# Optimization experiments

Hardware: AMD Instinct MI355X
Metric: run time of the kernel (lower is better)

The kernel has to match this reference:

```python
import jax, jax.numpy as jnp
import numpy as np

N = 100000      # nodes
E = 1600000     # edges (before self-loops)
F_IN = 16       # num_node_features
HID = 16        # hid
HEADS = 4       # in_head == out_head
B = 64          # num graphs
G = 16          # num_global_features
NEG_SLOPE = 0.2


def gat_conv(x, src, dst, W, a_src, a_dst, b, concat):
    """PyG-style GATConv. x:[N,F], W:[F,H*C], a_src/a_dst:[H,C], b:[H*C] or [C]."""
    n = x.shape[0]
    H, C = a_src.shape
    h = (x @ W).reshape(n, H, C)                       # [N,H,C]
    alpha_s = (h * a_src).sum(-1)                      # [N,H]
    alpha_d = (h * a_dst).sum(-1)                      # [N,H]
    e = jax.nn.leaky_relu(alpha_s[src] + alpha_d[dst], NEG_SLOPE)  # [E',H]
    # segment softmax over destination nodes (stable; max is grad-free)
    m = jax.lax.stop_gradient(jax.ops.segment_max(e, dst, num_segments=n))
    ex = jnp.exp(e - m[dst])
    denom = jax.ops.segment_sum(ex, dst, num_segments=n)
    alpha = ex / (denom[dst] + 1e-16)                  # [E',H]
    out = jax.ops.segment_sum(h[src] * alpha[:, :, None], dst, num_segments=n)  # [N,H,C]
    out = out.reshape(n, H * C) if concat else out.mean(axis=1)
    return out + b


def setup_inputs() -> dict:
    key = jax.random.key(0)
    ks = jax.random.split(key, 24)
    s = 0.1
    inp = {
        "x": jax.random.normal(ks[0], (N, F_IN), jnp.float32),
        "stats": jax.random.normal(ks[1], (B, G), jnp.float32),
        # conv1: F_IN -> HID, heads=HEADS, concat=True
        "W1": jax.random.normal(ks[2], (F_IN, HEADS * HID), jnp.float32) * s,
        "a1s": jax.random.normal(ks[3], (HEADS, HID), jnp.float32) * s,
        "a1d": jax.random.normal(ks[4], (HEADS, HID), jnp.float32) * s,
        "b1": jnp.zeros((HEADS * HID,), jnp.float32),
        # conv2: HID*HEADS -> HID, heads=HEADS, concat=False
        "W2": jax.random.normal(ks[5], (HEADS * HID, HEADS * HID), jnp.float32) * s,
        "a2s": jax.random.normal(ks[6], (HEADS, HID), jnp.float32) * s,
        "a2d": jax.random.normal(ks[7], (HEADS, HID), jnp.float32) * s,
        "b2": jnp.zeros((HID,), jnp.float32),
        # conv3: HID -> HID, heads=HEADS, concat=False
        "W3": jax.random.normal(ks[8], (HID, HEADS * HID), jnp.float32) * s,
        "a3s": jax.random.normal(ks[9], (HEADS, HID), jnp.float32) * s,
        "a3d": jax.random.normal(ks[10], (HEADS, HID), jnp.float32) * s,
        "b3": jnp.zeros((HID,), jnp.float32),
        # MLP head
        "fw1": jax.random.normal(ks[11], (HID + G, 32), jnp.float32) * s,
        "fb1": jnp.zeros((32,), jnp.float32),
        "fw2": jax.random.normal(ks[12], (32, 16), jnp.float32) * s,
        "fb2": jnp.zeros((16,), jnp.float32),
        "fw3": jax.random.normal(ks[13], (16, 1), jnp.float32) * s,
        "fb3": jnp.zeros((1,), jnp.float32),
        "edge_index": jax.random.randint(ks[14], (2, E), 0, N, jnp.int64),
        "batch": jnp.sort(jax.random.randint(ks[15], (N,), 0, B, jnp.int64)),
    }
    return inp


def reference(x, stats, W1, a1s, a1d, b1, W2, a2s, a2d, b2, W3, a3s, a3d, b3,
              fw1, fb1, fw2, fb2, fw3, fb3, edge_index, batch):
    n = x.shape[0]
    loops = jnp.arange(n, dtype=edge_index.dtype)
    src = jnp.concatenate([edge_index[0], loops])  # add_self_loops=True (PyG default)
    dst = jnp.concatenate([edge_index[1], loops])
    h = jax.nn.elu(gat_conv(x, src, dst, W1, a1s, a1d, b1, True))
    h = jax.nn.elu(gat_conv(h, src, dst, W2, a2s, a2d, b2, False))
    h = gat_conv(h, src, dst, W3, a3s, a3d, b3, False)
    nb = stats.shape[0]
    pooled = jax.ops.segment_sum(h, batch, num_segments=nb)
    counts = jax.ops.segment_sum(jnp.ones((n,), h.dtype), batch, num_segments=nb)
    pooled = pooled / jnp.maximum(counts, 1.0)[:, None]   # global_mean_pool
    z = jnp.concatenate([pooled, stats], axis=1)
    z = jax.nn.relu(z @ fw1 + fb1)
    z = jax.nn.relu(z @ fw2 + fb2)
    return z @ fw3 + fb3
```

## Files before the change

### kernel.cpp

```cpp
#include <hip/hip_runtime.h>
#include <hip/hip_bf16.h>
#include <hip/hip_fp16.h>

#define NNODES 100000
#define NEDGES 1600000
#define NB     64
#define NG     16
#define POOL_SLOTS (NB * NG + NB)

#define BKT_SHIFT 7
#define NPB 128
#define NBKT ((NNODES + NPB - 1) / NPB)
#define BCAP 4096
#define SCAT_BLOCKS 256
#define NL1_BLOCKS 2048
#define REC 128

typedef float vf2 __attribute__((ext_vector_type(2)));

__device__ __forceinline__ float leaky02(float v) {
    return v > 0.0f ? v : 0.2f * v;
}

__device__ __forceinline__ unsigned char cvt_fp8(float a) {
    int r = __builtin_amdgcn_cvt_pk_fp8_f32(a, a, 0, false);
    return (unsigned char)(r & 0xFF);
}

__device__ __forceinline__ float4 loadQ4(const unsigned char* p) {
    int u = *(const int*)p;
    vf2 lo = __builtin_amdgcn_cvt_pk_f32_fp8(u, false);
    vf2 hi = __builtin_amdgcn_cvt_pk_f32_fp8(u, true);
    return make_float4(lo.x, lo.y, hi.x, hi.y);
}

__device__ __forceinline__ void storeH4(__half* p, float4 v) {
    __half2 a = __floats2half2_rn(v.x, v.y);
    __half2 b = __floats2half2_rn(v.z, v.w);
    uint2 raw;
    raw.x = *reinterpret_cast<unsigned*>(&a);
    raw.y = *reinterpret_cast<unsigned*>(&b);
    *(uint2*)p = raw;
}

template <int FIN>
__device__ __forceinline__ void nl_body_f32(const float* __restrict__ X,
                                            const float* __restrict__ W,
                                            const float* __restrict__ a_s,
                                            const float* __restrict__ a_d,
                                            unsigned char* __restrict__ Hrec,
                                            float* __restrict__ AD, int n,
                                            int wave0, int nwaves, int lane) {
    int head = lane >> 4;
    float w[FIN];
#pragma unroll
    for (int k = 0; k < FIN; ++k) w[k] = W[k * 64 + lane];
    float asl = a_s[lane], adl = a_d[lane];

    for (int i = wave0; i < n; i += nwaves) {
        const float* __restrict__ xr = X + (size_t)i * FIN;
        float acc = 0.0f;
#pragma unroll
        for (int k = 0; k < FIN; ++k) acc += xr[k] * w[k];
        unsigned char* row = Hrec + (size_t)i * REC;
        row[lane] = cvt_fp8(acc);
        float s1 = acc * asl, s2 = acc * adl;
#pragma unroll
        for (int off = 1; off < 16; off <<= 1) {
            s1 += __shfl_xor(s1, off);
            s2 += __shfl_xor(s2, off);
        }
        if ((lane & 15) == 0) {
            ((float*)(row + 64))[head] = s1;
            AD[(size_t)i * 4 + head] = s2;
        }
    }
}

template <int FIN>
__global__ void node_linear3h(const unsigned* __restrict__ X,
                              const float* __restrict__ W,
                              const float* __restrict__ a_s,
                              const float* __restrict__ a_d,
                              unsigned char* __restrict__ Hrec,
                              float* __restrict__ AD, int n) {
    int lane = threadIdx.x & 63;
    int head = lane >> 4;
    int wave = __builtin_amdgcn_readfirstlane(
        (int)((blockIdx.x * blockDim.x + threadIdx.x) >> 6));
    int nwaves = (gridDim.x * blockDim.x) >> 6;

    float w[FIN];
#pragma unroll
    for (int k = 0; k < FIN; ++k) w[k] = W[k * 64 + lane];
    float asl = a_s[lane], adl = a_d[lane];

    for (int i = wave; i < n; i += nwaves) {
        const unsigned* __restrict__ xr = X + (size_t)i * (FIN / 2);
        float acc = 0.0f;
#pragma unroll
        for (int k = 0; k < FIN / 2; ++k) {
            unsigned u = xr[k];
            __half2 hh = *reinterpret_cast<const __half2*>(&u);
            float2 f = __half22float2(hh);
            acc += f.x * w[2 * k] + f.y * w[2 * k + 1];
        }
        unsigned char* row = Hrec + (size_t)i * REC;
        row[lane] = cvt_fp8(acc);
        float s1 = acc * asl, s2 = acc * adl;
#pragma unroll
        for (int off = 1; off < 16; off <<= 1) {
            s1 += __shfl_xor(s1, off);
            s2 += __shfl_xor(s2, off);
        }
        if ((lane & 15) == 0) {
            ((float*)(row + 64))[head] = s1;
            AD[(size_t)i * 4 + head] = s2;
        }
    }
}

__global__ void scatter_nl1(const int* __restrict__ src,
                            const int* __restrict__ dst,
                            int* __restrict__ bucketCnt,
                            unsigned int* __restrict__ pairs, int ne,
                            const float* __restrict__ X,
                            const float* __restrict__ W,
                            const float* __restrict__ a_s,
                            const float* __restrict__ a_d,
                            unsigned char* __restrict__ Hrec,
                            float* __restrict__ AD, int n) {
    __shared__ int hist[NBKT];
    __shared__ int base[NBKT];
    int tid = threadIdx.x;

    if (blockIdx.x >= SCAT_BLOCKS) {
        int lane = tid & 63;
        int wave = __builtin_amdgcn_readfirstlane(
            (int)(((blockIdx.x - SCAT_BLOCKS) * blockDim.x + tid) >> 6));
        int nwaves = (NL1_BLOCKS * 256) >> 6;
        nl_body_f32<16>(X, W, a_s, a_d, Hrec, AD, n, wave, nwaves, lane);
        return;
    }

    for (int i = tid; i < NBKT; i += 256) hist[i] = 0;
    __syncthreads();

    int chunk = (ne + SCAT_BLOCKS - 1) / SCAT_BLOCKS;
    int beg = blockIdx.x * chunk;
    int end = min(beg + chunk, ne);

    for (int e0 = beg; e0 < end; e0 += 1024) {
        int d[4];
#pragma unroll
        for (int q = 0; q < 4; ++q) {
            int e = e0 + q * 256 + tid;
            d[q] = (e < end) ? dst[e] : -1;
        }
#pragma unroll
        for (int q = 0; q < 4; ++q)
            if (d[q] >= 0) atomicAdd(&hist[d[q] >> BKT_SHIFT], 1);
    }
    __syncthreads();

    for (int i = tid; i < NBKT; i += 256) {
        int h = hist[i];
        base[i] = h ? atomicAdd(&bucketCnt[i], h) : 0;
        hist[i] = 0;
    }
    __syncthreads();

    for (int e0 = beg; e0 < end; e0 += 1024) {
        int d[4], s[4];
#pragma unroll
        for (int q = 0; q < 4; ++q) {
            int e = e0 + q * 256 + tid;
            d[q] = (e < end) ? dst[e] : -1;
            s[q] = (e < end) ? src[e] : 0;
        }
        int r[4], bkt[4];
#pragma unroll
        for (int q = 0; q < 4; ++q) {
            if (d[q] >= 0) {
                bkt[q] = d[q] >> BKT_SHIFT;
                r[q] = base[bkt[q]] + atomicAdd(&hist[bkt[q]], 1);
            }
        }
#pragma unroll
        for (int q = 0; q < 4; ++q) {
            if (d[q] >= 0 && r[q] < BCAP)
                pairs[(size_t)bkt[q] * BCAP + r[q]] =
                    (unsigned)s[q] | ((unsigned)(d[q] & (NPB - 1)) << 20);
        }
    }
}

__global__ void bucket_sort(const unsigned int* __restrict__ pairs,
                            const int* __restrict__ bucketCnt,
                            int* __restrict__ srcs,
                            int* __restrict__ indptr, int n) {
    __shared__ int hist[NPB];
    __shared__ int offl[NPB];
    __shared__ int cur[NPB];
    __shared__ int red[256];
    __shared__ int lsrc[BCAP];
    int bkt = blockIdx.x;
    int t = threadIdx.x;
    int cnt = min(bucketCnt[bkt], BCAP);

    int partial = 0;
    for (int j = t; j < bkt; j += 256) partial += min(bucketCnt[j], BCAP);
    red[t] = partial;
    if (t < NPB) hist[t] = 0;
    __syncthreads();
    for (int s = 128; s > 0; s >>= 1) {
        if (t < s) red[t] += red[t + s];
        __syncthreads();
    }
    int boff = red[0];
    if (bkt == NBKT - 1 && t == 0) indptr[n] = boff + cnt;

    const unsigned int* __restrict__ p = pairs + (size_t)bkt * BCAP;
    unsigned int v[BCAP / 256];
#pragma unroll
    for (int i = 0; i < BCAP / 256; ++i) {
        int e = i * 256 + t;
        v[i] = 0u;
        if (e < cnt) {
            v[i] = p[e];
            atomicAdd(&hist[v[i] >> 20], 1);
        }
    }
    __syncthreads();
    if (t < NPB) offl[t] = hist[t];
    __syncthreads();
    for (int off = 1; off < NPB; off <<= 1) {
        int x = 0;
        if (t < NPB && t >= off) x = offl[t - off];
        __syncthreads();
        if (t < NPB && t >= off) offl[t] += x;
        __syncthreads();
    }
    if (t < NPB) {
        int ex = offl[t] - hist[t];
        cur[t] = ex;
        int node = bkt * NPB + t;
        if (node < n) indptr[node] = boff + ex;
    }
    __syncthreads();
#pragma unroll
    for (int i = 0; i < BCAP / 256; ++i) {
        int e = i * 256 + t;
        if (e < cnt) {
            int r = atomicAdd(&cur[v[i] >> 20], 1);
            lsrc[r] = (int)(v[i] & 0xFFFFFu);
        }
    }
    __syncthreads();
    for (int e = t; e < cnt; e += 256) srcs[boff + e] = lsrc[e];
}

__device__ __forceinline__ float4 gat_agg_core(
    const unsigned char* __restrict__ Hrec, const float* __restrict__ AD,
    const int* __restrict__ indptr, const int* __restrict__ srcs,
    int d, int grp, int sl, int head) {
    const unsigned char* __restrict__ rowD = Hrec + (size_t)d * REC;
    float ad  = AD[(size_t)d * 4 + head];
    float asd = *(const float*)(rowD + 64 + 4 * head);
    float t0 = asd + ad;
    float wself = __expf(leaky02(t0));
    float den = wself;
    float4 h4s = loadQ4(rowD + sl * 4);
    float4 acc = make_float4(wself * h4s.x, wself * h4s.y,
                             wself * h4s.z, wself * h4s.w);

    int beg = indptr[d], end = indptr[d + 1];
    for (int e0 = beg; e0 < end; e0 += 16) {
        int cnt = min(16, end - e0);
        int myS = (sl < cnt) ? srcs[e0 + sl] : 0;
        int j = 0;
        for (; j + 4 <= cnt; j += 4) {
            const unsigned char* r[4];
            float a[4]; float4 h4[4];
#pragma unroll
            for (int q = 0; q < 4; ++q) {
                int s = __shfl(myS, (grp << 4) + j + q);
                r[q] = Hrec + (size_t)s * REC;
            }
#pragma unroll
            for (int q = 0; q < 4; ++q)
                a[q] = *(const float*)(r[q] + 64 + 4 * head);
#pragma unroll
            for (int q = 0; q < 4; ++q) h4[q] = loadQ4(r[q] + sl * 4);
#pragma unroll
            for (int q = 0; q < 4; ++q) {
                float t = a[q] + ad;
                float w = __expf(leaky02(t));
                den += w;
                acc.x += w * h4[q].x; acc.y += w * h4[q].y;
                acc.z += w * h4[q].z; acc.w += w * h4[q].w;
            }
        }
        for (; j < cnt; ++j) {
            int s = __shfl(myS, (grp << 4) + j);
            const unsigned char* rr = Hrec + (size_t)s * REC;
            float t = *(const float*)(rr + 64 + 4 * head) + ad;
            float w = __expf(leaky02(t));
            float4 h4 = loadQ4(rr + sl * 4);
            den += w;
            acc.x += w * h4.x; acc.y += w * h4.y;
            acc.z += w * h4.z; acc.w += w * h4.w;
        }
    }
    float inv = 1.0f / (den + 1e-16f);
    return make_float4(acc.x * inv, acc.y * inv, acc.z * inv, acc.w * inv);
}

__global__ void gat_pull_l1(const unsigned char* __restrict__ Hrec,
                            const float* __restrict__ AD,
                            const int* __restrict__ indptr,
                            const int* __restrict__ srcs,
                            const float* __restrict__ bias,
                            __half* __restrict__ out, int n) {
    int lane = threadIdx.x & 63;
    int grp = lane >> 4, sl = lane & 15, head = sl >> 2;
    int wave = (blockIdx.x * blockDim.x + threadIdx.x) >> 6;
    int nwaves = (gridDim.x * blockDim.x) >> 6;
    for (int d0 = wave * 4; d0 < n; d0 += nwaves * 4) {
        int d = d0 + grp;
        if (d < n) {
            float4 v = gat_agg_core(Hrec, AD, indptr, srcs, d, grp, sl, head);
            float4 b4 = *(const float4*)(bias + sl * 4);
            v.x += b4.x; v.y += b4.y; v.z += b4.z; v.w += b4.w;
            v.x = v.x > 0.f ? v.x : __expf(v.x) - 1.f;
            v.y = v.y > 0.f ? v.y : __expf(v.y) - 1.f;
            v.z = v.z > 0.f ? v.z : __expf(v.z) - 1.f;
            v.w = v.w > 0.f ? v.w : __expf(v.w) - 1.f;
            storeH4(out + (size_t)d * 64 + sl * 4, v);
        }
    }
}

__global__ void gat_pull_l2(const unsigned char* __restrict__ Hrec,
                            float* __restrict__ AD,
                            const int* __restrict__ indptr,
                            const int* __restrict__ srcs,
                            const float* __restrict__ bias,
                            const float* __restrict__ W3,
                            const float* __restrict__ a3s,
                            const float* __restrict__ a3d,
                            unsigned char* __restrict__ Hout, int n) {
    __shared__ float w3s[16 * 64];
    for (int i = threadIdx.x; i < 16 * 64; i += 256) w3s[i] = W3[i];
    __syncthreads();

    int lane = threadIdx.x & 63;
    int grp = lane >> 4, sl = lane & 15, head = sl >> 2;
    int wave = (blockIdx.x * blockDim.x + threadIdx.x) >> 6;
    int nwaves = (gridDim.x * blockDim.x) >> 6;
    float4 as4 = *(const float4*)(a3s + head * 16 + (sl & 3) * 4);
    float4 ad4 = *(const float4*)(a3d + head * 16 + (sl & 3) * 4);
    float4 b4  = *(const float4*)(bias + (sl & 3) * 4);

    for (int d0 = wave * 4; d0 < n; d0 += nwaves * 4) {
        int d = d0 + grp;
        if (d < n) {
            float4 v = gat_agg_core(Hrec, AD, indptr, srcs, d, grp, sl, head);
#pragma unroll
            for (int off = 4; off <= 8; off <<= 1) {
                v.x += __shfl_xor(v.x, off);
                v.y += __shfl_xor(v.y, off);
                v.z += __shfl_xor(v.z, off);
                v.w += __shfl_xor(v.w, off);
            }
            v.x = 0.25f * v.x + b4.x; v.y = 0.25f * v.y + b4.y;
            v.z = 0.25f * v.z + b4.z; v.w = 0.25f * v.w + b4.w;
            v.x = v.x > 0.f ? v.x : __expf(v.x) - 1.f;
            v.y = v.y > 0.f ? v.y : __expf(v.y) - 1.f;
            v.z = v.z > 0.f ? v.z : __expf(v.z) - 1.f;
            v.w = v.w > 0.f ? v.w : __expf(v.w) - 1.f;

            float xin[16];
#pragma unroll
            for (int q = 0; q < 4; ++q) {
                int srcl = (grp << 4) + q;
                xin[4 * q + 0] = __shfl(v.x, srcl);
                xin[4 * q + 1] = __shfl(v.y, srcl);
                xin[4 * q + 2] = __shfl(v.z, srcl);
                xin[4 * q + 3] = __shfl(v.w, srcl);
            }
            float4 o = make_float4(0.f, 0.f, 0.f, 0.f);
#pragma unroll
            for (int k = 0; k < 16; ++k) {
                float4 wr = *(const float4*)&w3s[k * 64 + 4 * sl];
                o.x += xin[k] * wr.x; o.y += xin[k] * wr.y;
                o.z += xin[k] * wr.z; o.w += xin[k] * wr.w;
            }
            unsigned char* rowO = Hout + (size_t)d * REC;
            int pk = __builtin_amdgcn_cvt_pk_fp8_f32(o.x, o.y, 0, false);
            pk = __builtin_amdgcn_cvt_pk_fp8_f32(o.z, o.w, pk, true);
            *(int*)(rowO + 4 * sl) = pk;
            float s1 = o.x * as4.x + o.y * as4.y + o.z * as4.z + o.w * as4.w;
            float s2 = o.x * ad4.x + o.y * ad4.y + o.z * ad4.z + o.w * ad4.w;
            s1 += __shfl_xor(s1, 1); s1 += __shfl_xor(s1, 2);
            s2 += __shfl_xor(s2, 1); s2 += __shfl_xor(s2, 2);
            if ((sl & 3) == 0) {
                ((float*)(rowO + 64))[head] = s1;
                AD[(size_t)d * 4 + head] = s2;
            }
        }
    }
}

__global__ void gat_pull_l3(const unsigned char* __restrict__ Hrec,
                            const float* __restrict__ AD,
                            const int* __restrict__ indptr,
                            const int* __restrict__ srcs,
                            const float* __restrict__ bias,
                            const int* __restrict__ batch,
                            float* __restrict__ PC, int n) {
    __shared__ float lp[POOL_SLOTS];
    for (int i = threadIdx.x; i < POOL_SLOTS; i += 256) lp[i] = 0.f;
    __syncthreads();

    int lane = threadIdx.x & 63;
    int grp = lane >> 4, sl = lane & 15, head = sl >> 2;
    int wave = (blockIdx.x * blockDim.x + threadIdx.x) >> 6;
    int nwaves = (gridDim.x * blockDim.x) >> 6;
    float4 b4 = *(const float4*)(bias + (sl & 3) * 4);

    for (int d0 = wave * 4; d0 < n; d0 += nwaves * 4) {
        int d = d0 + grp;
        if (d < n) {
            float4 v = gat_agg_core(Hrec, AD, indptr, srcs, d, grp, sl, head);
#pragma unroll
            for (int off = 4; off <= 8; off <<= 1) {
                v.x += __shfl_xor(v.x, off);
                v.y += __shfl_xor(v.y, off);
                v.z += __shfl_xor(v.z, off);
                v.w += __shfl_xor(v.w, off);
            }
            v.x = 0.25f * v.x + b4.x; v.y = 0.25f * v.y + b4.y;
            v.z = 0.25f * v.z + b4.z; v.w = 0.25f * v.w + b4.w;
            if (sl < 4) {
                int b = batch[d];
                atomicAdd(&lp[b * 16 + sl * 4 + 0], v.x);
                atomicAdd(&lp[b * 16 + sl * 4 + 1], v.y);
                atomicAdd(&lp[b * 16 + sl * 4 + 2], v.z);
                atomicAdd(&lp[b * 16 + sl * 4 + 3], v.w);
                if (sl == 0) atomicAdd(&lp[NB * NG + b], 1.0f);
            }
        }
    }
    __syncthreads();
    for (int i = threadIdx.x; i < POOL_SLOTS; i += 256) {
        float s = lp[i];
        if (s != 0.f) atomicAdd(&PC[i], s);
    }
}

__global__ void mlp_head(const float* __restrict__ pooled_counts,
                         const float* __restrict__ stats,
                         const float* __restrict__ fw1, const float* __restrict__ fb1,
                         const float* __restrict__ fw2, const float* __restrict__ fb2,
                         const float* __restrict__ fw3, const float* __restrict__ fb3,
                         float* __restrict__ out) {
    int g = threadIdx.x;
    if (g >= NB) return;
    const float* pooled = pooled_counts;
    const float* counts = pooled_counts + NB * NG;
    float z[32];
    float inv = 1.0f / fmaxf(counts[g], 1.0f);
#pragma unroll
    for (int c = 0; c < 16; ++c) z[c] = pooled[g * 16 + c] * inv;
#pragma unroll
    for (int c = 0; c < 16; ++c) z[16 + c] = stats[g * 16 + c];

    float z1[32];
#pragma unroll
    for (int j = 0; j < 32; ++j) {
        float acc = fb1[j];
        for (int k = 0; k < 32; ++k) acc += z[k] * fw1[k * 32 + j];
        z1[j] = fmaxf(acc, 0.0f);
    }
    float z2[16];
#pragma unroll
    for (int j = 0; j < 16; ++j) {
        float acc = fb2[j];
        for (int k = 0; k < 32; ++k) acc += z1[k] * fw2[k * 16 + j];
        z2[j] = fmaxf(acc, 0.0f);
    }
    float acc = fb3[0];
#pragma unroll
    for (int k = 0; k < 16; ++k) acc += z2[k] * fw3[k];
    out[g] = acc;
}

extern "C" void kernel_launch(void* const* d_in, const int* in_sizes, int n_in,
                              void* d_out, int out_size, void* d_ws, size_t ws_size,
                              hipStream_t stream) {
    const float* x    = (const float*)d_in[0];
    const float* stats= (const float*)d_in[1];
    const float* W1   = (const float*)d_in[2];
    const float* a1s  = (const float*)d_in[3];
    const float* a1d  = (const float*)d_in[4];
    const float* b1   = (const float*)d_in[5];
    const float* W2   = (const float*)d_in[6];
    const float* a2s  = (const float*)d_in[7];
    const float* a2d  = (const float*)d_in[8];
    const float* b2   = (const float*)d_in[9];
    const float* W3   = (const float*)d_in[10];
    const float* a3s  = (const float*)d_in[11];
    const float* a3d  = (const float*)d_in[12];
    const float* b3   = (const float*)d_in[13];
    const float* fw1  = (const float*)d_in[14];
    const float* fb1  = (const float*)d_in[15];
    const float* fw2  = (const float*)d_in[16];
    const float* fb2  = (const float*)d_in[17];
    const float* fw3  = (const float*)d_in[18];
    const float* fb3  = (const float*)d_in[19];
    const int* ei     = (const int*)d_in[20];
    const int* batch  = (const int*)d_in[21];

    const int n = NNODES, ne = NEDGES;
    const int* srcI = ei;
    const int* dstI = ei + ne;

    unsigned char* HqA = (unsigned char*)d_ws;
    unsigned char* HqB = HqA + (size_t)n * REC;
    float* AD   = (float*)(HqB + (size_t)n * REC);
    float* PC   = AD + (size_t)n * 4;
    int* bucketCnt = (int*)(PC + POOL_SLOTS);
    int* indptr    = bucketCnt + NBKT;
    int* srcs      = indptr + (n + 1);
    size_t off = (size_t)((char*)(srcs + ne) - (char*)d_ws);
    off = (off + 255) & ~(size_t)255;
    unsigned int* pairs = (unsigned int*)((char*)d_ws + off);
    __half* B16 = (__half*)pairs;

    const int TB = 256;
    const int nlBlocks   = 2048;
    const int pullBlocks = (n + 15) / 16;

    hipMemsetAsync(PC, 0, (POOL_SLOTS + NBKT) * sizeof(int), stream);

    scatter_nl1<<<SCAT_BLOCKS + NL1_BLOCKS, TB, 0, stream>>>(
        srcI, dstI, bucketCnt, pairs, ne,
        x, W1, a1s, a1d, HqA, AD, n);
    bucket_sort<<<NBKT, TB, 0, stream>>>(pairs, bucketCnt, srcs, indptr, n);

    gat_pull_l1<<<pullBlocks, TB, 0, stream>>>(HqA, AD, indptr, srcs, b1, B16, n);

    node_linear3h<64><<<nlBlocks, TB, 0, stream>>>((const unsigned*)B16, W2,
                                                   a2s, a2d, HqA, AD, n);
    gat_pull_l2<<<pullBlocks, TB, 0, stream>>>(HqA, AD, indptr, srcs, b2,
                                               W3, a3s, a3d, HqB, n);
    gat_pull_l3<<<pullBlocks, TB, 0, stream>>>(HqB, AD, indptr, srcs, b3,
                                               batch, PC, n);

    mlp_head<<<1, 64, 0, stream>>>(PC, stats, fw1, fb1, fw2, fb2, fw3, fb3,
                                   (float*)d_out);
}
```

Before: 331.1 us.

## Split node records into packed fp8 features and separate alpha arrays, deepen gather unroll

Result: slower. 395.9 us (+19.6%).

```diff
diff --git a/kernel.cpp b/kernel.cpp
--- a/kernel.cpp
+++ b/kernel.cpp
@@ -14,7 +14,6 @@
 #define BCAP 4096
 #define SCAT_BLOCKS 256
 #define NL1_BLOCKS 2048
-#define REC 128
 
 typedef float vf2 __attribute__((ext_vector_type(2)));
 
@@ -48,7 +47,8 @@
                                             const float* __restrict__ W,
                                             const float* __restrict__ a_s,
                                             const float* __restrict__ a_d,
-                                            unsigned char* __restrict__ Hrec,
+                                            unsigned char* __restrict__ H,
+                                            float* __restrict__ AS,
                                             float* __restrict__ AD, int n,
                                             int wave0, int nwaves, int lane) {
     int head = lane >> 4;
@@ -62,8 +62,7 @@
         float acc = 0.0f;
 #pragma unroll
         for (int k = 0; k < FIN; ++k) acc += xr[k] * w[k];
-        unsigned char* row = Hrec + (size_t)i * REC;
-        row[lane] = cvt_fp8(acc);
+        H[(size_t)i * 64 + lane] = cvt_fp8(acc);
         float s1 = acc * asl, s2 = acc * adl;
 #pragma unroll
         for (int off = 1; off < 16; off <<= 1) {
@@ -71,7 +70,7 @@
             s2 += __shfl_xor(s2, off);
         }
         if ((lane & 15) == 0) {
-            ((float*)(row + 64))[head] = s1;
+            AS[(size_t)i * 4 + head] = s1;
             AD[(size_t)i * 4 + head] = s2;
         }
     }
@@ -82,7 +81,8 @@
                               const float* __restrict__ W,
                               const float* __restrict__ a_s,
                               const float* __restrict__ a_d,
-                              unsigned char* __restrict__ Hrec,
+                              unsigned char* __restrict__ H,
+                              float* __restrict__ AS,
                               float* __restrict__ AD, int n) {
     int lane = threadIdx.x & 63;
     int head = lane >> 4;
@@ -105,8 +105,7 @@
             float2 f = __half22float2(hh);
             acc += f.x * w[2 * k] + f.y * w[2 * k + 1];
         }
-        unsigned char* row = Hrec + (size_t)i * REC;
-        row[lane] = cvt_fp8(acc);
+        H[(size_t)i * 64 + lane] = cvt_fp8(acc);
         float s1 = acc * asl, s2 = acc * adl;
 #pragma unroll
         for (int off = 1; off < 16; off <<= 1) {
@@ -114,7 +113,7 @@
             s2 += __shfl_xor(s2, off);
         }
         if ((lane & 15) == 0) {
-            ((float*)(row + 64))[head] = s1;
+            AS[(size_t)i * 4 + head] = s1;
             AD[(size_t)i * 4 + head] = s2;
         }
     }
@@ -128,7 +127,8 @@
                             const float* __restrict__ W,
                             const float* __restrict__ a_s,
                             const float* __restrict__ a_d,
-                            unsigned char* __restrict__ Hrec,
+                            unsigned char* __restrict__ H,
+                            float* __restrict__ AS,
                             float* __restrict__ AD, int n) {
     __shared__ int hist[NBKT];
     __shared__ int base[NBKT];
@@ -139,7 +139,7 @@
         int wave = __builtin_amdgcn_readfirstlane(
             (int)(((blockIdx.x - SCAT_BLOCKS) * blockDim.x + tid) >> 6));
         int nwaves = (NL1_BLOCKS * 256) >> 6;
-        nl_body_f32<16>(X, W, a_s, a_d, Hrec, AD, n, wave, nwaves, lane);
+        nl_body_f32<16>(X, W, a_s, a_d, H, AS, AD, n, wave, nwaves, lane);
         return;
     }
 
@@ -155,7 +155,7 @@
 #pragma unroll
         for (int q = 0; q < 4; ++q) {
             int e = e0 + q * 256 + tid;
-            d[q] = (e < end) ? dst[e] : -1;
+            d[q] = (e < end) ? __builtin_nontemporal_load(dst + e) : -1;
         }
 #pragma unroll
         for (int q = 0; q < 4; ++q)
@@ -175,8 +175,8 @@
 #pragma unroll
         for (int q = 0; q < 4; ++q) {
             int e = e0 + q * 256 + tid;
-            d[q] = (e < end) ? dst[e] : -1;
-            s[q] = (e < end) ? src[e] : 0;
+            d[q] = (e < end) ? __builtin_nontemporal_load(dst + e) : -1;
+            s[q] = (e < end) ? __builtin_nontemporal_load(src + e) : 0;
         }
         int r[4], bkt[4];
 #pragma unroll
@@ -189,8 +189,9 @@
 #pragma unroll
         for (int q = 0; q < 4; ++q) {
             if (d[q] >= 0 && r[q] < BCAP)
-                pairs[(size_t)bkt[q] * BCAP + r[q]] =
-                    (unsigned)s[q] | ((unsigned)(d[q] & (NPB - 1)) << 20);
+                __builtin_nontemporal_store(
+                    (unsigned)s[q] | ((unsigned)(d[q] & (NPB - 1)) << 20),
+                    pairs + (size_t)bkt[q] * BCAP + r[q]);
         }
     }
 }
@@ -227,7 +228,7 @@
         int e = i * 256 + t;
         v[i] = 0u;
         if (e < cnt) {
-            v[i] = p[e];
+            v[i] = __builtin_nontemporal_load(p + e);
             atomicAdd(&hist[v[i] >> 20], 1);
         }
     }
@@ -261,37 +262,58 @@
 }
 
 __device__ __forceinline__ float4 gat_agg_core(
-    const unsigned char* __restrict__ Hrec, const float* __restrict__ AD,
+    const unsigned char* __restrict__ H, const float* __restrict__ AS,
+    const float* __restrict__ AD,
     const int* __restrict__ indptr, const int* __restrict__ srcs,
     int d, int grp, int sl, int head) {
-    const unsigned char* __restrict__ rowD = Hrec + (size_t)d * REC;
+    int beg = indptr[d], end = indptr[d + 1];
+    int myS = 0;
+    if (beg < end && sl < min(16, end - beg))
+        myS = __builtin_nontemporal_load(srcs + beg + sl);
+
     float ad  = AD[(size_t)d * 4 + head];
-    float asd = *(const float*)(rowD + 64 + 4 * head);
+    float asd = AS[(size_t)d * 4 + head];
     float t0 = asd + ad;
     float wself = __expf(leaky02(t0));
     float den = wself;
-    float4 h4s = loadQ4(rowD + sl * 4);
+    float4 h4s = loadQ4(H + (size_t)d * 64 + sl * 4);
     float4 acc = make_float4(wself * h4s.x, wself * h4s.y,
                              wself * h4s.z, wself * h4s.w);
 
-    int beg = indptr[d], end = indptr[d + 1];
     for (int e0 = beg; e0 < end; e0 += 16) {
         int cnt = min(16, end - e0);
-        int myS = (sl < cnt) ? srcs[e0 + sl] : 0;
         int j = 0;
+        for (; j + 8 <= cnt; j += 8) {
+            int s[8]; float a[8]; float4 h4[8];
+#pragma unroll
+            for (int q = 0; q < 8; ++q)
+                s[q] = __shfl(myS, (grp << 4) + j + q);
+#pragma unroll
+            for (int q = 0; q < 8; ++q)
+                a[q] = AS[(size_t)s[q] * 4 + head];
+#pragma unroll
+            for (int q = 0; q < 8; ++q)
+                h4[q] = loadQ4(H + (size_t)s[q] * 64 + sl * 4);
+#pragma unroll
+            for (int q = 0; q < 8; ++q) {
+                float t = a[q] + ad;
+                float w = __expf(leaky02(t));
+                den += w;
+                acc.x += w * h4[q].x; acc.y += w * h4[q].y;
+                acc.z += w * h4[q].z; acc.w += w * h4[q].w;
+            }
+        }
         for (; j + 4 <= cnt; j += 4) {
-            const unsigned char* r[4];
-            float a[4]; float4 h4[4];
-#pragma unroll
-            for (int q = 0; q < 4; ++q) {
-                int s = __shfl(myS, (grp << 4) + j + q);
-                r[q] = Hrec + (size_t)s * REC;
-            }
+            int s[4]; float a[4]; float4 h4[4];
 #pragma unroll
             for (int q = 0; q < 4; ++q)
-                a[q] = *(const float*)(r[q] + 64 + 4 * head);
-#pragma unroll
-            for (int q = 0; q < 4; ++q) h4[q] = loadQ4(r[q] + sl * 4);
+                s[q] = __shfl(myS, (grp << 4) + j + q);
+#pragma unroll
+            for (int q = 0; q < 4; ++q)
+                a[q] = AS[(size_t)s[q] * 4 + head];
+#pragma unroll
+            for (int q = 0; q < 4; ++q)
+                h4[q] = loadQ4(H + (size_t)s[q] * 64 + sl * 4);
 #pragma unroll
             for (int q = 0; q < 4; ++q) {
                 float t = a[q] + ad;
@@ -303,20 +325,23 @@
         }
         for (; j < cnt; ++j) {
             int s = __shfl(myS, (grp << 4) + j);
-            const unsigned char* rr = Hrec + (size_t)s * REC;
-            float t = *(const float*)(rr + 64 + 4 * head) + ad;
+            float t = AS[(size_t)s * 4 + head] + ad;
             float w = __expf(leaky02(t));
-            float4 h4 = loadQ4(rr + sl * 4);
+            float4 h4 = loadQ4(H + (size_t)s * 64 + sl * 4);
             den += w;
             acc.x += w * h4.x; acc.y += w * h4.y;
             acc.z += w * h4.z; acc.w += w * h4.w;
         }
+        int nb = e0 + 16;
+        if (nb < end && sl < min(16, end - nb))
+            myS = __builtin_nontemporal_load(srcs + nb + sl);
     }
     float inv = 1.0f / (den + 1e-16f);
     return make_float4(acc.x * inv, acc.y * inv, acc.z * inv, acc.w * inv);
 }
 
-__global__ void gat_pull_l1(const unsigned char* __restrict__ Hrec,
+__global__ void gat_pull_l1(const unsigned char* __restrict__ H,
+                            const float* __restrict__ AS,
                             const float* __restrict__ AD,
                             const int* __restrict__ indptr,
                             const int* __restrict__ srcs,
@@ -329,7 +354,7 @@
     for (int d0 = wave * 4; d0 < n; d0 += nwaves * 4) {
         int d = d0 + grp;
         if (d < n) {
-            float4 v = gat_agg_core(Hrec, AD, indptr, srcs, d, grp, sl, head);
+            float4 v = gat_agg_core(H, AS, AD, indptr, srcs, d, grp, sl, head);
             float4 b4 = *(const float4*)(bias + sl * 4);
             v.x += b4.x; v.y += b4.y; v.z += b4.z; v.w += b4.w;
             v.x = v.x > 0.f ? v.x : __expf(v.x) - 1.f;
@@ -341,7 +366,8 @@
     }
 }
 
-__global__ void gat_pull_l2(const unsigned char* __restrict__ Hrec,
+__global__ void gat_pull_l2(const unsigned char* __restrict__ H,
+                            const float* __restrict__ AS,
                             float* __restrict__ AD,
                             const int* __restrict__ indptr,
                             const int* __restrict__ srcs,
@@ -349,7 +375,8 @@
                             const float* __restrict__ W3,
                             const float* __restrict__ a3s,
                             const float* __restrict__ a3d,
-                            unsigned char* __restrict__ Hout, int n) {
+                            unsigned char* __restrict__ Hout,
+                            float* __restrict__ ASout, int n) {
     __shared__ float w3s[16 * 64];
     for (int i = threadIdx.x; i < 16 * 64; i += 256) w3s[i] = W3[i];
     __syncthreads();
@@ -365,7 +392,7 @@
     for (int d0 = wave * 4; d0 < n; d0 += nwaves * 4) {
         int d = d0 + grp;
         if (d < n) {
-            float4 v = gat_agg_core(Hrec, AD, indptr, srcs, d, grp, sl, head);
+            float4 v = gat_agg_core(H, AS, AD, indptr, srcs, d, grp, sl, head);
 #pragma unroll
             for (int off = 4; off <= 8; off <<= 1) {
                 v.x += __shfl_xor(v.x, off);
@@ -396,23 +423,23 @@
                 o.x += xin[k] * wr.x; o.y += xin[k] * wr.y;
                 o.z += xin[k] * wr.z; o.w += xin[k] * wr.w;
             }
-            unsigned char* rowO = Hout + (size_t)d * REC;
             int pk = __builtin_amdgcn_cvt_pk_fp8_f32(o.x, o.y, 0, false);
             pk = __builtin_amdgcn_cvt_pk_fp8_f32(o.z, o.w, pk, true);
-            *(int*)(rowO + 4 * sl) = pk;
+            *(int*)(Hout + (size_t)d * 64 + 4 * sl) = pk;
             float s1 = o.x * as4.x + o.y * as4.y + o.z * as4.z + o.w * as4.w;
             float s2 = o.x * ad4.x + o.y * ad4.y + o.z * ad4.z + o.w * ad4.w;
             s1 += __shfl_xor(s1, 1); s1 += __shfl_xor(s1, 2);
             s2 += __shfl_xor(s2, 1); s2 += __shfl_xor(s2, 2);
             if ((sl & 3) == 0) {
-                ((float*)(rowO + 64))[head] = s1;
+                ASout[(size_t)d * 4 + head] = s1;
                 AD[(size_t)d * 4 + head] = s2;
             }
         }
     }
 }
 
-__global__ void gat_pull_l3(const unsigned char* __restrict__ Hrec,
+__global__ void gat_pull_l3(const unsigned char* __restrict__ H,
+                            const float* __restrict__ AS,
                             const float* __restrict__ AD,
                             const int* __restrict__ indptr,
                             const int* __restrict__ srcs,
@@ -432,7 +459,7 @@
     for (int d0 = wave * 4; d0 < n; d0 += nwaves * 4) {
         int d = d0 + grp;
         if (d < n) {
-            float4 v = gat_agg_core(Hrec, AD, indptr, srcs, d, grp, sl, head);
+            float4 v = gat_agg_core(H, AS, AD, indptr, srcs, d, grp, sl, head);
 #pragma unroll
             for (int off = 4; off <= 8; off <<= 1) {
                 v.x += __shfl_xor(v.x, off);
@@ -527,8 +554,10 @@
     const int* dstI = ei + ne;
 
     unsigned char* HqA = (unsigned char*)d_ws;
-    unsigned char* HqB = HqA + (size_t)n * REC;
-    float* AD   = (float*)(HqB + (size_t)n * REC);
+    unsigned char* HqB = HqA + (size_t)n * 64;
+    float* ASa  = (float*)(HqB + (size_t)n * 64);
+    float* ASb  = ASa + (size_t)n * 4;
+    float* AD   = ASb + (size_t)n * 4;
     float* PC   = AD + (size_t)n * 4;
     int* bucketCnt = (int*)(PC + POOL_SLOTS);
     int* indptr    = bucketCnt + NBKT;
@@ -546,16 +575,17 @@
 
     scatter_nl1<<<SCAT_BLOCKS + NL1_BLOCKS, TB, 0, stream>>>(
         srcI, dstI, bucketCnt, pairs, ne,
-        x, W1, a1s, a1d, HqA, AD, n);
+        x, W1, a1s, a1d, HqA, ASa, AD, n);
     bucket_sort<<<NBKT, TB, 0, stream>>>(pairs, bucketCnt, srcs, indptr, n);
 
-    gat_pull_l1<<<pullBlocks, TB, 0, stream>>>(HqA, AD, indptr, srcs, b1, B16, n);
+    gat_pull_l1<<<pullBlocks, TB, 0, stream>>>(HqA, ASa, AD, indptr, srcs, b1,
+                                               B16, n);
 
     node_linear3h<64><<<nlBlocks, TB, 0, stream>>>((const unsigned*)B16, W2,
-                                                   a2s, a2d, HqA, AD, n);
-    gat_pull_l2<<<pullBlocks, TB, 0, stream>>>(HqA, AD, indptr, srcs, b2,
-                                               W3, a3s, a3d, HqB, n);
-    gat_pull_l3<<<pullBlocks, TB, 0, stream>>>(HqB, AD, indptr, srcs, b3,
+                                                   a2s, a2d, HqA, ASa, AD, n);
+    gat_pull_l2<<<pullBlocks, TB, 0, stream>>>(HqA, ASa, AD, indptr, srcs, b2,
+                                               W3, a3s, a3d, HqB, ASb, n);
+    gat_pull_l3<<<pullBlocks, TB, 0, stream>>>(HqB, ASb, AD, indptr, srcs, b3,
                                                batch, PC, n);
 
     mlp_head<<<1, 64, 0, stream>>>(PC, stats, fw1, fb1, fw2, fb2, fw3, fb3,
```
